# Performance work log

Hardware: AMD Instinct MI355X
Metric: run time of the kernel (lower is better)

Reference implementation:

```python
import jax, jax.numpy as jnp
import numpy as np

B, NQ, NK, D = 8, 2048, 2048, 256


def setup_inputs() -> dict:
    key = jax.random.key(0)
    ks = jax.random.split(key, 4)
    scale = 1.0 / np.sqrt(D)
    return {
        "query": jax.random.normal(ks[0], (B, NQ, D), dtype=jnp.float32),
        "key": jax.random.normal(ks[1], (B, NK, D), dtype=jnp.float32),
        "Wq": jax.random.normal(ks[2], (D, D), dtype=jnp.float32) * scale,
        "bq": jnp.zeros((D,), dtype=jnp.float32),
        "Wk": jax.random.normal(ks[3], (D, D), dtype=jnp.float32) * scale,
        "bk": jnp.zeros((D,), dtype=jnp.float32),
    }


def reference(query, key, Wq, bq, Wk, bk):
    # value = key (pre-projection), as in the torch module
    value = key
    # FFT over the sequence axis (dim=1), keep real part
    q = jnp.real(jnp.fft.fft(query, axis=1)).astype(query.dtype)
    # torch nn.Linear: y = x @ W.T + b
    q = q @ Wq.T + bq                      # [B, NQ, D]
    k = key @ Wk.T + bk                    # [B, NK, D]
    scale = 1.0 / jnp.sqrt(jnp.asarray(q.shape[-1], q.dtype))
    scores = jnp.einsum('bqd,bkd->bqk', q, k) * scale   # [B, NQ, NK]
    probs = jax.nn.softmax(scores, axis=-1)
    out = jnp.einsum('bqk,bkd->bqd', probs, value)       # [B, NQ, D]
    return out
```

## Files before the change

kernel.cpp:

```cpp
#include <hip/hip_runtime.h>

#define B_ 8
#define NQ_ 2048
#define NK_ 2048
#define D_ 256
#define KF_ 1056

typedef __attribute__((ext_vector_type(8))) short bf16x8_t;
typedef __attribute__((ext_vector_type(4))) float f32x4_t;

static __device__ __forceinline__ unsigned short f2bf(float x) {
  unsigned int u = __float_as_uint(x);
  unsigned int r = (u + 0x7FFFu + ((u >> 16) & 1u)) >> 16;
  return (unsigned short)r;
}
static __device__ __forceinline__ float bf2f(unsigned short b) {
  return __uint_as_float(((unsigned int)b) << 16);
}

typedef __attribute__((address_space(1))) unsigned int gas_u32;
typedef __attribute__((address_space(3))) unsigned int las_u32;
static __device__ __forceinline__ void gl16(const void* g, void* l) {
  __builtin_amdgcn_global_load_lds((const gas_u32*)g, (las_u32*)l, 16, 0, 0);
}

__global__ __launch_bounds__(256) void split_kernel(const float* __restrict__ x,
                                                    unsigned short* __restrict__ xh,
                                                    unsigned short* __restrict__ xl,
                                                    int n) {
  const int i = blockIdx.x * 256 + threadIdx.x;
  if (i < n) {
    const float v = x[i];
    const unsigned short hb = f2bf(v);
    xh[i] = hb;
    xl[i] = f2bf(v - bf2f(hb));
  }
}

__global__ __launch_bounds__(256) void cos_split_kernel(unsigned short* __restrict__ Ch,
                                                        unsigned short* __restrict__ Cl) {
  const int idx = blockIdx.x * 256 + threadIdx.x;
  const int i = idx / KF_, n = idx % KF_;
  float c = 0.f;
  if (n <= 1024) {
    const int m = (i * n) & 2047;
    c = cosf((float)m * 0.0030679615757712823f);
  }
  const unsigned short hb = f2bf(c);
  Ch[idx] = hb;
  Cl[idx] = f2bf(c - bf2f(hb));
}

__global__ __launch_bounds__(256) void qtf_split_kernel(const float* __restrict__ q,
                                                        unsigned short* __restrict__ Qtfh,
                                                        unsigned short* __restrict__ Qtfl) {
  __shared__ float lds[32][33];
  const int t  = threadIdx.x;
  const int n0 = blockIdx.x * 32;
  const int d0 = blockIdx.y * 32;
  const int b  = blockIdx.z;
#pragma unroll
  for (int p = 0; p < 4; ++p) {
    const int idx = t + 256 * p;
    const int dd = idx & 31, nn = idx >> 5;
    const int n = n0 + nn;
    float v = 0.f;
    if (n <= 1024) v = q[((size_t)b * NQ_ + n) * D_ + d0 + dd];
    if (n >= 1 && n <= 1023) v += q[((size_t)b * NQ_ + (2048 - n)) * D_ + d0 + dd];
    lds[nn][dd] = v;
  }
  __syncthreads();
#pragma unroll
  for (int p = 0; p < 4; ++p) {
    const int idx = t + 256 * p;
    const int nn = idx & 31, dd = idx >> 5;
    const float v = lds[nn][dd];
    const unsigned short hb = f2bf(v);
    const size_t o = ((size_t)b * D_ + d0 + dd) * KF_ + n0 + nn;
    Qtfh[o] = hb;
    Qtfl[o] = f2bf(v - bf2f(hb));
  }
}

__global__ __launch_bounds__(256) void vt_bf16_kernel(const unsigned short* __restrict__ keyh,
                                                      unsigned short* __restrict__ Vt) {
  __shared__ unsigned short lds[32][40];
  const int t  = threadIdx.x;
  const int j0 = blockIdx.x * 32;
  const int d0 = blockIdx.y * 32;
  const int b  = blockIdx.z;
#pragma unroll
  for (int p = 0; p < 4; ++p) {
    const int idx = t + 256 * p;
    const int dd = idx & 31, jj = idx >> 5;
    lds[jj][dd] = keyh[((size_t)b * NK_ + j0 + jj) * D_ + d0 + dd];
  }
  __syncthreads();
#pragma unroll
  for (int p = 0; p < 4; ++p) {
    const int idx = t + 256 * p;
    const int jj = idx & 31, dd = idx >> 5;
    Vt[((size_t)b * D_ + d0 + dd) * NK_ + j0 + jj] = lds[jj][dd];
  }
}

__global__ __launch_bounds__(256, 2) void dft_mfma(const unsigned short* __restrict__ Ch,
                                                   const unsigned short* __restrict__ Cl,
                                                   const unsigned short* __restrict__ Qtfh,
                                                   const unsigned short* __restrict__ Qtfl,
                                                   float* __restrict__ qr) {
  __shared__ __align__(16) unsigned short Ah[128][40];
  __shared__ __align__(16) unsigned short Al[128][40];
  __shared__ __align__(16) unsigned short Bh[128][40];
  __shared__ __align__(16) unsigned short Bl[128][40];
  const int t = threadIdx.x;
  const int b = blockIdx.z / 3, split = blockIdx.z % 3;
  const int i0 = blockIdx.x * 128, d0 = blockIdx.y * 128;
  const int w = t >> 6, lane = t & 63, quad = lane >> 4, l16 = lane & 15;
  const int wq = w & 1, wj = w >> 1;
  float* qrs = qr + (size_t)split * ((size_t)B_ * 1152 * D_);

  f32x4_t acc[4][4];
#pragma unroll
  for (int a = 0; a < 4; ++a)
#pragma unroll
    for (int c = 0; c < 4; ++c) acc[a][c] = (f32x4_t)0.f;

  const size_t abase = (size_t)i0 * KF_;
  const size_t bbase = ((size_t)b * D_ + d0) * KF_;

  for (int c0 = split * 352; c0 < split * 352 + 352; c0 += 32) {
#pragma unroll
    for (int it = 0; it < 2; ++it) {
      const int unit = t + 256 * it;
      const int row = unit >> 2, u = (unit & 3) * 8;
      const size_t go = (size_t)row * KF_ + c0 + u;
      *(uint4*)&Ah[row][u] = *(const uint4*)&Ch[abase + go];
      *(uint4*)&Al[row][u] = *(const uint4*)&Cl[abase + go];
      *(uint4*)&Bh[row][u] = *(const uint4*)&Qtfh[bbase + go];
      *(uint4*)&Bl[row][u] = *(const uint4*)&Qtfl[bbase + go];
    }
    __syncthreads();
    {
      const int dcol = quad * 8;
      bf16x8_t ah[4], al[4], bh[4], bl[4];
#pragma unroll
      for (int x = 0; x < 4; ++x) {
        ah[x] = *(const bf16x8_t*)&Ah[wq * 64 + x * 16 + l16][dcol];
        al[x] = *(const bf16x8_t*)&Al[wq * 64 + x * 16 + l16][dcol];
        bh[x] = *(const bf16x8_t*)&Bh[wj * 64 + x * 16 + l16][dcol];
        bl[x] = *(const bf16x8_t*)&Bl[wj * 64 + x * 16 + l16][dcol];
      }
#pragma unroll
      for (int at = 0; at < 4; ++at)
#pragma unroll
        for (int jt = 0; jt < 4; ++jt) {
          acc[at][jt] = __builtin_amdgcn_mfma_f32_16x16x32_bf16(ah[at], bh[jt], acc[at][jt], 0, 0, 0);
          acc[at][jt] = __builtin_amdgcn_mfma_f32_16x16x32_bf16(ah[at], bl[jt], acc[at][jt], 0, 0, 0);
          acc[at][jt] = __builtin_amdgcn_mfma_f32_16x16x32_bf16(al[at], bh[jt], acc[at][jt], 0, 0, 0);
        }
    }
    __syncthreads();
  }
#pragma unroll
  for (int at = 0; at < 4; ++at) {
#pragma unroll
    for (int jt = 0; jt < 4; ++jt) {
      const int d = d0 + wj * 64 + jt * 16 + l16;
#pragma unroll
      for (int r = 0; r < 4; ++r) {
        const int i = i0 + wq * 64 + at * 16 + quad * 4 + r;
        qrs[((size_t)b * 1152 + i) * D_ + d] = acc[at][jt][r];
      }
    }
  }
}

__global__ __launch_bounds__(256) void qr_finalize_kernel(const float* __restrict__ qr,
                                                          unsigned short* __restrict__ qrh,
                                                          unsigned short* __restrict__ qrl) {
  const int i = blockIdx.x, b = blockIdx.y, d = threadIdx.x;
  const int src = (i <= 1087) ? i : (2048 - i);
  const size_t S = (size_t)B_ * 1152 * D_;
  const size_t idx = ((size_t)b * 1152 + src) * D_ + d;
  const float v = qr[idx] + qr[idx + S] + qr[idx + 2 * S];
  const unsigned short hb = f2bf(v);
  const size_t o = ((size_t)b * NQ_ + i) * D_ + d;
  qrh[o] = hb;
  qrl[o] = f2bf(v - bf2f(hb));
}

__global__ __launch_bounds__(256, 2) void proj_mfma(const unsigned short* __restrict__ xh,
                                                    const unsigned short* __restrict__ xl,
                                                    const unsigned short* __restrict__ Wh,
                                                    const unsigned short* __restrict__ Wl,
                                                    const float* __restrict__ bias,
                                                    unsigned short* __restrict__ yh,
                                                    unsigned short* __restrict__ yl) {
  __shared__ __align__(16) unsigned short Xh[128][72];
  __shared__ __align__(16) unsigned short Xl[128][72];
  __shared__ __align__(16) unsigned short Bh[128][72];
  __shared__ __align__(16) unsigned short Bl[128][72];
  const int t = threadIdx.x;
  const int m0 = blockIdx.x * 128, o0 = blockIdx.y * 128;
  const int w = t >> 6, lane = t & 63, quad = lane >> 4, l16 = lane & 15;
  const int wq = w & 1, wj = w >> 1;

  f32x4_t acc[4][4];
#pragma unroll
  for (int a = 0; a < 4; ++a)
#pragma unroll
    for (int c = 0; c < 4; ++c) acc[a][c] = (f32x4_t)0.f;

  const size_t xbase = (size_t)m0 * D_;
  const size_t wbase = (size_t)o0 * D_;

  for (int c0 = 0; c0 < D_; c0 += 64) {
#pragma unroll
    for (int it = 0; it < 4; ++it) {
      const int unit = t + 256 * it;
      const int row = unit >> 3, u = (unit & 7) * 8;
      const size_t go = (size_t)row * D_ + c0 + u;
      *(uint4*)&Xh[row][u] = *(const uint4*)&xh[xbase + go];
      *(uint4*)&Xl[row][u] = *(const uint4*)&xl[xbase + go];
      *(uint4*)&Bh[row][u] = *(const uint4*)&Wh[wbase + go];
      *(uint4*)&Bl[row][u] = *(const uint4*)&Wl[wbase + go];
    }
    __syncthreads();
#pragma unroll
    for (int ks = 0; ks < 2; ++ks) {
      const int dcol = ks * 32 + quad * 8;
      bf16x8_t ah[4], al[4], bh[4], bl[4];
#pragma unroll
      for (int x = 0; x < 4; ++x) {
        ah[x] = *(const bf16x8_t*)&Xh[wq * 64 + x * 16 + l16][dcol];
        al[x] = *(const bf16x8_t*)&Xl[wq * 64 + x * 16 + l16][dcol];
        bh[x] = *(const bf16x8_t*)&Bh[wj * 64 + x * 16 + l16][dcol];
        bl[x] = *(const bf16x8_t*)&Bl[wj * 64 + x * 16 + l16][dcol];
      }
#pragma unroll
      for (int at = 0; at < 4; ++at)
#pragma unroll
        for (int jt = 0; jt < 4; ++jt) {
          acc[at][jt] = __builtin_amdgcn_mfma_f32_16x16x32_bf16(ah[at], bh[jt], acc[at][jt], 0, 0, 0);
          acc[at][jt] = __builtin_amdgcn_mfma_f32_16x16x32_bf16(ah[at], bl[jt], acc[at][jt], 0, 0, 0);
          acc[at][jt] = __builtin_amdgcn_mfma_f32_16x16x32_bf16(al[at], bh[jt], acc[at][jt], 0, 0, 0);
        }
    }
    __syncthreads();
  }
#pragma unroll
  for (int at = 0; at < 4; ++at) {
#pragma unroll
    for (int jt = 0; jt < 4; ++jt) {
      const int o = o0 + wj * 64 + jt * 16 + l16;
      const float bv = bias[o];
#pragma unroll
      for (int r = 0; r < 4; ++r) {
        const int m = m0 + wq * 64 + at * 16 + quad * 4 + r;
        const float v = acc[at][jt][r] + bv;
        const unsigned short hb = f2bf(v);
        yh[(size_t)m * D_ + o] = hb;
        yl[(size_t)m * D_ + o] = f2bf(v - bf2f(hb));
      }
    }
  }
}

__global__ __launch_bounds__(512, 4) void scores_p(const unsigned short* __restrict__ qh,
                                                   const unsigned short* __restrict__ ql,
                                                   const unsigned short* __restrict__ kh,
                                                   const unsigned short* __restrict__ kl,
                                                   unsigned short* __restrict__ Pb,
                                                   float2* __restrict__ stat) {
  __shared__ __align__(16) unsigned short Qh[128][64];
  __shared__ __align__(16) unsigned short Ql[128][64];
  __shared__ __align__(16) unsigned short Kh[128][64];
  __shared__ __align__(16) unsigned short Kl[128][64];
  __shared__ float mred[2][128];
  __shared__ float lred[2][128];
  const int t = threadIdx.x;
  const int b = blockIdx.z;
  const int i0 = blockIdx.x * 128, j0 = blockIdx.y * 128;
  const int jb = blockIdx.y;
  const int w = t >> 6, lane = t & 63, quad = lane >> 4, l16 = lane & 15;
  const int wq = w & 3, wj = w >> 2;
  const int sr0 = t >> 3, ssl = t & 7;

  f32x4_t acc[2][4];
#pragma unroll
  for (int x = 0; x < 2; ++x)
#pragma unroll
    for (int y = 0; y < 4; ++y) acc[x][y] = (f32x4_t)0.f;

  const size_t qbase = ((size_t)b * NQ_ + i0) * D_;
  const size_t kbase = ((size_t)b * NK_ + j0) * D_;

  auto STAGE = [&](int c0) {
#pragma unroll
    for (int half = 0; half < 2; ++half) {
      const int row = half * 64 + sr0;
      const int sg = (ssl ^ (row & 7)) * 8;
      const size_t ro = (size_t)row * D_ + c0 + sg;
      gl16(qh + qbase + ro, &Qh[half * 64 + w * 8][0]);
      gl16(ql + qbase + ro, &Ql[half * 64 + w * 8][0]);
      gl16(kh + kbase + ro, &Kh[half * 64 + w * 8][0]);
      gl16(kl + kbase + ro, &Kl[half * 64 + w * 8][0]);
    }
  };

  STAGE(0);

#pragma unroll
  for (int s = 0; s < 4; ++s) {
    asm volatile("s_waitcnt vmcnt(0)" ::: "memory");
    __builtin_amdgcn_s_barrier();
    asm volatile("" ::: "memory");

#pragma unroll
    for (int ks = 0; ks < 2; ++ks) {
      bf16x8_t ah[2], al[2], bh[4], bl[4];
#pragma unroll
      for (int x = 0; x < 2; ++x) {
        const int ar = wq * 32 + x * 16 + l16;
        const int asl = ((ks * 4 + quad) ^ (ar & 7)) * 8;
        ah[x] = *(const bf16x8_t*)&Qh[ar][asl];
        al[x] = *(const bf16x8_t*)&Ql[ar][asl];
      }
#pragma unroll
      for (int y = 0; y < 4; ++y) {
        const int br = wj * 64 + y * 16 + l16;
        const int bsl = ((ks * 4 + quad) ^ (br & 7)) * 8;
        bh[y] = *(const bf16x8_t*)&Kh[br][bsl];
        bl[y] = *(const bf16x8_t*)&Kl[br][bsl];
      }
#pragma unroll
      for (int x = 0; x < 2; ++x)
#pragma unroll
        for (int y = 0; y < 4; ++y) {
          acc[x][y] = __builtin_amdgcn_mfma_f32_16x16x32_bf16(ah[x], bh[y], acc[x][y], 0, 0, 0);
          acc[x][y] = __builtin_amdgcn_mfma_f32_16x16x32_bf16(ah[x], bl[y], acc[x][y], 0, 0, 0);
          acc[x][y] = __builtin_amdgcn_mfma_f32_16x16x32_bf16(al[x], bh[y], acc[x][y], 0, 0, 0);
        }
    }

    asm volatile("" ::: "memory");
    __builtin_amdgcn_s_barrier();
    asm volatile("" ::: "memory");
    if (s < 3) STAGE((s + 1) * 64);
  }

  const float scale = 0.0625f;
  float mt[2][4];
#pragma unroll
  for (int x = 0; x < 2; ++x)
#pragma unroll
    for (int r = 0; r < 4; ++r) mt[x][r] = -3e38f;
#pragma unroll
  for (int x = 0; x < 2; ++x)
#pragma unroll
    for (int y = 0; y < 4; ++y)
#pragma unroll
      for (int r = 0; r < 4; ++r) {
        acc[x][y][r] *= scale;
        mt[x][r] = fmaxf(mt[x][r], acc[x][y][r]);
      }
#pragma unroll
  for (int off = 1; off < 16; off <<= 1)
#pragma unroll
    for (int x = 0; x < 2; ++x)
#pragma unroll
      for (int r = 0; r < 4; ++r) mt[x][r] = fmaxf(mt[x][r], __shfl_xor(mt[x][r], off));
  if (l16 == 0) {
#pragma unroll
    for (int x = 0; x < 2; ++x)
#pragma unroll
      for (int r = 0; r < 4; ++r)
        mred[wj][wq * 32 + x * 16 + quad * 4 + r] = mt[x][r];
  }
  __syncthreads();
  float nrow[2][4], mu[2][4], lt[2][4];
#pragma unroll
  for (int x = 0; x < 2; ++x)
#pragma unroll
    for (int r = 0; r < 4; ++r) {
      const int rr = wq * 32 + x * 16 + quad * 4 + r;
      const float m = fmaxf(mred[0][rr], mred[1][rr]);
      const float n = ceilf(m * 1.44269504f);
      nrow[x][r] = n;
      mu[x][r] = n * 0.69314718056f;
      lt[x][r] = 0.f;
    }
  const size_t pbase = ((size_t)(b * 16 + jb)) * NQ_ * 128;
#pragma unroll
  for (int x = 0; x < 2; ++x)
#pragma unroll
    for (int y = 0; y < 4; ++y) {
      const int jloc = wj * 64 + y * 16 + l16;
#pragma unroll
      for (int r = 0; r < 4; ++r) {
        const int i = i0 + wq * 32 + x * 16 + quad * 4 + r;
        float p = __expf(acc[x][y][r] - mu[x][r]);
        p = fmaxf(p, 8.673617e-19f);
        lt[x][r] += p;
        Pb[pbase + (size_t)i * 128 + jloc] = f2bf(p);
      }
    }
#pragma unroll
  for (int off = 1; off < 16; off <<= 1)
#pragma unroll
    for (int x = 0; x < 2; ++x)
#pragma unroll
      for (int r = 0; r < 4; ++r) lt[x][r] += __shfl_xor(lt[x][r], off);
  if (l16 == 0) {
#pragma unroll
    for (int x = 0; x < 2; ++x)
#pragma unroll
      for (int r = 0; r < 4; ++r)
        lred[wj][wq * 32 + x * 16 + quad * 4 + r] = lt[x][r];
  }
  __syncthreads();
  if (wj == 0 && l16 == 0) {
#pragma unroll
    for (int x = 0; x < 2; ++x)
#pragma unroll
      for (int r = 0; r < 4; ++r) {
        const int rr = wq * 32 + x * 16 + quad * 4 + r;
        stat[(size_t)jb * (B_ * NQ_) + (size_t)b * NQ_ + i0 + rr] =
            make_float2(nrow[x][r], lred[0][rr] + lred[1][rr]);
      }
  }
}

__global__ __launch_bounds__(256) void rowfin_kernel(const float2* __restrict__ stat,
                                                     float2* __restrict__ srow) {
  const int i = blockIdx.x * 256 + threadIdx.x;
  float2 st[16];
  float m = -3e38f;
#pragma unroll
  for (int jb = 0; jb < 16; ++jb) {
    st[jb] = stat[(size_t)jb * (B_ * NQ_) + i];
    m = fmaxf(m, st[jb].x);
  }
  float l = 0.f;
#pragma unroll
  for (int jb = 0; jb < 16; ++jb) l += st[jb].y * exp2f(st[jb].x - m);
  srow[i] = make_float2(m, 1.0f / l);
}

__global__ __launch_bounds__(512, 1) void pv_p(const unsigned short* __restrict__ Pb,
                                               const float2* __restrict__ stat,
                                               const float2* __restrict__ srow,
                                               const unsigned short* __restrict__ Vt,
                                               float* __restrict__ out) {
  __shared__ __align__(16) unsigned short Ps[3][64][64];
  __shared__ __align__(16) unsigned short Vs[3][256][64];
  const int t = threadIdx.x;
  const int lb = (blockIdx.x & 7) * 32 + (blockIdx.x >> 3);
  const int mb = lb * 64;
  const int b  = lb >> 5;
  const int i0 = mb & (NQ_ - 1);
  const int w = t >> 6, lane = t & 63, quad = lane >> 4, l16 = lane & 15;
  const int wm = w & 1, wd = w >> 1;
  const int prow = t >> 3, pslot = t & 7;

  unsigned int es2[16][2];
  {
    float nmax[2];
#pragma unroll
    for (int x = 0; x < 2; ++x)
      nmax[x] = srow[mb + wm * 32 + x * 16 + l16].x;
#pragma unroll
    for (int jb = 0; jb < 16; ++jb)
#pragma unroll
      for (int x = 0; x < 2; ++x) {
        const int arow = mb + wm * 32 + x * 16 + l16;
        int e = (int)(nmax[x] - stat[(size_t)jb * (B_ * NQ_) + arow].x);
        e = e < 0 ? 0 : (e > 60 ? 60 : e);
        es2[jb][x] = (unsigned int)(e << 7) * 0x00010001u;
      }
  }

  f32x4_t acc[2][4];
#pragma unroll
  for (int x = 0; x < 2; ++x)
#pragma unroll
    for (int y = 0; y < 4; ++y) acc[x][y] = (f32x4_t)0.f;

  const size_t vbase = (size_t)b * D_ * (size_t)NK_;

  auto STAGE = [&](int nb, int s) {
    const int jj = s * 64;
    const int jb = jj >> 7, off = jj & 127;
    {
      const int sg = pslot ^ (prow & 7);
      gl16(Pb + ((size_t)(b * 16 + jb)) * NQ_ * 128 +
               (size_t)(i0 + prow) * 128 + off + sg * 8,
           &Ps[nb][w * 8][0]);
    }
#pragma unroll
    for (int k = 0; k < 4; ++k) {
      const int vrow = k * 64 + prow;
      const int sg = pslot ^ (vrow & 7);
      gl16(Vt + vbase + (size_t)vrow * NK_ + jj + sg * 8,
           &Vs[nb][k * 64 + w * 8][0]);
    }
  };

  asm volatile("s_waitcnt vmcnt(0)" ::: "memory");
  STAGE(0, 0);
  STAGE(1, 1);

#pragma unroll
  for (int s = 0; s < 32; ++s) {
    const int cb = s % 3;
    if (s < 30) {
      STAGE((s + 2) % 3, s + 2);
      asm volatile("s_waitcnt vmcnt(10)" ::: "memory");
    } else if (s == 30) {
      asm volatile("s_waitcnt vmcnt(5)" ::: "memory");
    } else {
      asm volatile("s_waitcnt vmcnt(0)" ::: "memory");
    }
    __builtin_amdgcn_s_barrier();
    asm volatile("" ::: "memory");

    const unsigned int e0 = es2[s >> 1][0], e1 = es2[s >> 1][1];
#pragma unroll
    for (int ks = 0; ks < 2; ++ks) {
      bf16x8_t a[2], bv[4];
#pragma unroll
      for (int x = 0; x < 2; ++x) {
        const int row = wm * 32 + x * 16 + l16;
        const int sk = (ks * 4 + quad) ^ (row & 7);
        uint4 u = *(const uint4*)&Ps[cb][row][sk * 8];
        const unsigned int e = (x == 0) ? e0 : e1;
        u.x -= e; u.y -= e; u.z -= e; u.w -= e;
        a[x] = *(const bf16x8_t*)&u;
      }
#pragma unroll
      for (int y = 0; y < 4; ++y) {
        const int row = wd * 64 + y * 16 + l16;
        const int sk = (ks * 4 + quad) ^ (row & 7);
        bv[y] = *(const bf16x8_t*)&Vs[cb][row][sk * 8];
      }
#pragma unroll
      for (int x = 0; x < 2; ++x)
#pragma unroll
        for (int y = 0; y < 4; ++y)
          acc[x][y] = __builtin_amdgcn_mfma_f32_16x16x32_bf16(a[x], bv[y], acc[x][y], 0, 0, 0);
    }

    asm volatile("" ::: "memory");
    __builtin_amdgcn_s_barrier();
    asm volatile("" ::: "memory");
  }

#pragma unroll
  for (int x = 0; x < 2; ++x) {
    float sy[4];
#pragma unroll
    for (int r = 0; r < 4; ++r)
      sy[r] = srow[mb + wm * 32 + x * 16 + quad * 4 + r].y;
#pragma unroll
    for (int y = 0; y < 4; ++y) {
      const int d = wd * 64 + y * 16 + l16;
#pragma unroll
      for (int r = 0; r < 4; ++r) {
        const int m = mb + wm * 32 + x * 16 + quad * 4 + r;
        out[(size_t)m * D_ + d] = acc[x][y][r] * sy[r];
      }
    }
  }
}

extern "C" void kernel_launch(void* const* d_in, const int* in_sizes, int n_in,
                              void* d_out, int out_size, void* d_ws, size_t ws_size,
                              hipStream_t stream) {
  const float* query = (const float*)d_in[0];
  const float* key   = (const float*)d_in[1];
  const float* Wq    = (const float*)d_in[2];
  const float* bq    = (const float*)d_in[3];
  const float* Wk    = (const float*)d_in[4];
  const float* bk    = (const float*)d_in[5];
  float* out = (float*)d_out;

  char* ws = (char*)d_ws;
  const size_t MB = (size_t)1 << 20;
  unsigned short* qh = (unsigned short*)(ws);
  unsigned short* ql = (unsigned short*)(ws + 8 * MB);
  unsigned short* kh = (unsigned short*)(ws + 16 * MB);
  unsigned short* kl = (unsigned short*)(ws + 24 * MB);
  unsigned short* Vt = (unsigned short*)(ws + 32 * MB);
  unsigned short* Pb = (unsigned short*)(ws + 40 * MB);
  float2* stat = (float2*)(ws + 108 * MB);
  float2* srow = (float2*)(ws + 110 * MB);
  unsigned short* Ch   = (unsigned short*)(ws + 40 * MB);
  unsigned short* Cl   = (unsigned short*)(ws + 43 * MB);
  unsigned short* Qtfh = (unsigned short*)(ws + 46 * MB);
  unsigned short* Qtfl = (unsigned short*)(ws + 51 * MB);
  float*          qr   = (float*)(ws + 56 * MB);
  unsigned short* qrh  = (unsigned short*)(ws + 40 * MB);
  unsigned short* qrl  = (unsigned short*)(ws + 48 * MB);
  unsigned short* keyh = (unsigned short*)(ws + 92 * MB);
  unsigned short* keyl = (unsigned short*)(ws + 100 * MB);
  unsigned short* Wqh  = (unsigned short*)(ws + 111 * MB);
  unsigned short* Wql  = (unsigned short*)(ws + 111 * MB + 256 * 1024);
  unsigned short* Wkh  = (unsigned short*)(ws + 111 * MB + 512 * 1024);
  unsigned short* Wkl  = (unsigned short*)(ws + 111 * MB + 768 * 1024);

  dim3 blk(256);

  split_kernel<<<B_ * NK_ * D_ / 256, blk, 0, stream>>>(key, keyh, keyl, B_ * NK_ * D_);
  split_kernel<<<D_ * D_ / 256, blk, 0, stream>>>(Wq, Wqh, Wql, D_ * D_);
  split_kernel<<<D_ * D_ / 256, blk, 0, stream>>>(Wk, Wkh, Wkl, D_ * D_);
  cos_split_kernel<<<1152 * KF_ / 256, blk, 0, stream>>>(Ch, Cl);
  qtf_split_kernel<<<dim3(KF_ / 32, D_ / 32, B_), blk, 0, stream>>>(query, Qtfh, Qtfl);
  dft_mfma<<<dim3(9, 2, B_ * 3), blk, 0, stream>>>(Ch, Cl, Qtfh, Qtfl, qr);
  qr_finalize_kernel<<<dim3(2048, B_), blk, 0, stream>>>(qr, qrh, qrl);
  proj_mfma<<<dim3(B_ * NQ_ / 128, 2), blk, 0, stream>>>(qrh, qrl, Wqh, Wql, bq, qh, ql);
  proj_mfma<<<dim3(B_ * NK_ / 128, 2), blk, 0, stream>>>(keyh, keyl, Wkh, Wkl, bk, kh, kl);
  vt_bf16_kernel<<<dim3(NK_ / 32, D_ / 32, B_), blk, 0, stream>>>(keyh, Vt);
  scores_p<<<dim3(NQ_ / 128, NK_ / 128, B_), dim3(512), 0, stream>>>(qh, ql, kh, kl, Pb, stat);
  rowfin_kernel<<<B_ * NQ_ / 256, blk, 0, stream>>>(stat, srow);
  pv_p<<<dim3(256), dim3(512), 0, stream>>>(Pb, stat, srow, Vt, out);
}
```

Baseline: 206.7 us.

## Widen scores tile to 128x256 with interleaved hi/lo LDS staging

The scores kernel now computes a 128x256 tile per block instead of 128x128, halving the grid along the key axis. Each wave owns a 64x64 sub-tile with 16 accumulators, which raises MFMA work per LDS fragment load. The hi and lo bf16 halves are packed into one swizzled LDS row, and the K dimension is staged in 32-wide chunks over 8 steps. Statistics are still written per 128-column block so downstream kernels are unchanged. The larger tile increases register pressure under launch_bounds(512,4), which may spill or lower occupancy, and the grid shrinks to 1024 blocks.

```diff
diff --git a/kernel.cpp b/kernel.cpp
--- a/kernel.cpp
+++ b/kernel.cpp
@@ -273,161 +273,157 @@
                                                    const unsigned short* __restrict__ kl,
                                                    unsigned short* __restrict__ Pb,
                                                    float2* __restrict__ stat) {
-  __shared__ __align__(16) unsigned short Qh[128][64];
-  __shared__ __align__(16) unsigned short Ql[128][64];
-  __shared__ __align__(16) unsigned short Kh[128][64];
-  __shared__ __align__(16) unsigned short Kl[128][64];
-  __shared__ float mred[2][128];
-  __shared__ float lred[2][128];
+  __shared__ __align__(16) unsigned short Qhl[128][64];
+  __shared__ __align__(16) unsigned short Khl[256][64];
+  __shared__ float mred[4][128];
+  __shared__ float lred[4][128];
   const int t = threadIdx.x;
   const int b = blockIdx.z;
-  const int i0 = blockIdx.x * 128, j0 = blockIdx.y * 128;
-  const int jb = blockIdx.y;
+  const int i0 = blockIdx.x * 128, j0 = blockIdx.y * 256;
+  const int jb0 = blockIdx.y * 2;
   const int w = t >> 6, lane = t & 63, quad = lane >> 4, l16 = lane & 15;
-  const int wq = w & 3, wj = w >> 2;
-  const int sr0 = t >> 3, ssl = t & 7;
-
-  f32x4_t acc[2][4];
-#pragma unroll
-  for (int x = 0; x < 2; ++x)
-#pragma unroll
-    for (int y = 0; y < 4; ++y) acc[x][y] = (f32x4_t)0.f;
+  const int wq = w & 1, wj = w >> 1;
+  const int jbl = wj >> 1;
+
+  f32x4_t acc[4][4];
+#pragma unroll
+  for (int a = 0; a < 4; ++a)
+#pragma unroll
+    for (int c = 0; c < 4; ++c) acc[a][c] = (f32x4_t)0.f;
 
   const size_t qbase = ((size_t)b * NQ_ + i0) * D_;
   const size_t kbase = ((size_t)b * NK_ + j0) * D_;
 
   auto STAGE = [&](int c0) {
 #pragma unroll
-    for (int half = 0; half < 2; ++half) {
-      const int row = half * 64 + sr0;
-      const int sg = (ssl ^ (row & 7)) * 8;
-      const size_t ro = (size_t)row * D_ + c0 + sg;
-      gl16(qh + qbase + ro, &Qh[half * 64 + w * 8][0]);
-      gl16(ql + qbase + ro, &Ql[half * 64 + w * 8][0]);
-      gl16(kh + kbase + ro, &Kh[half * 64 + w * 8][0]);
-      gl16(kl + kbase + ro, &Kl[half * 64 + w * 8][0]);
+    for (int cp = 0; cp < 2; ++cp) {
+      const int r = w * 16 + cp * 8 + (lane >> 3);
+      const int lg = (lane & 7) ^ (r & 7);
+      const unsigned short* src = (lg < 4) ? qh : ql;
+      gl16(src + qbase + (size_t)r * D_ + c0 + (lg & 3) * 8,
+           &Qhl[w * 16 + cp * 8][0]);
+    }
+#pragma unroll
+    for (int cp = 0; cp < 4; ++cp) {
+      const int r = w * 32 + cp * 8 + (lane >> 3);
+      const int lg = (lane & 7) ^ (r & 7);
+      const unsigned short* src = (lg < 4) ? kh : kl;
+      gl16(src + kbase + (size_t)r * D_ + c0 + (lg & 3) * 8,
+           &Khl[w * 32 + cp * 8][0]);
     }
   };
 
   STAGE(0);
 
 #pragma unroll
-  for (int s = 0; s < 4; ++s) {
+  for (int s = 0; s < 8; ++s) {
     asm volatile("s_waitcnt vmcnt(0)" ::: "memory");
     __builtin_amdgcn_s_barrier();
     asm volatile("" ::: "memory");
 
-#pragma unroll
-    for (int ks = 0; ks < 2; ++ks) {
-      bf16x8_t ah[2], al[2], bh[4], bl[4];
-#pragma unroll
-      for (int x = 0; x < 2; ++x) {
-        const int ar = wq * 32 + x * 16 + l16;
-        const int asl = ((ks * 4 + quad) ^ (ar & 7)) * 8;
-        ah[x] = *(const bf16x8_t*)&Qh[ar][asl];
-        al[x] = *(const bf16x8_t*)&Ql[ar][asl];
-      }
-#pragma unroll
-      for (int y = 0; y < 4; ++y) {
-        const int br = wj * 64 + y * 16 + l16;
-        const int bsl = ((ks * 4 + quad) ^ (br & 7)) * 8;
-        bh[y] = *(const bf16x8_t*)&Kh[br][bsl];
-        bl[y] = *(const bf16x8_t*)&Kl[br][bsl];
-      }
-#pragma unroll
-      for (int x = 0; x < 2; ++x)
-#pragma unroll
-        for (int y = 0; y < 4; ++y) {
-          acc[x][y] = __builtin_amdgcn_mfma_f32_16x16x32_bf16(ah[x], bh[y], acc[x][y], 0, 0, 0);
-          acc[x][y] = __builtin_amdgcn_mfma_f32_16x16x32_bf16(ah[x], bl[y], acc[x][y], 0, 0, 0);
-          acc[x][y] = __builtin_amdgcn_mfma_f32_16x16x32_bf16(al[x], bh[y], acc[x][y], 0, 0, 0);
-        }
-    }
+    bf16x8_t ah[4], al[4], bh[4], bl[4];
+#pragma unroll
+    for (int x = 0; x < 4; ++x) {
+      const int ar = wq * 64 + x * 16 + l16;
+      ah[x] = *(const bf16x8_t*)&Qhl[ar][(quad ^ (ar & 7)) * 8];
+      al[x] = *(const bf16x8_t*)&Qhl[ar][((4 + quad) ^ (ar & 7)) * 8];
+      const int br = wj * 64 + x * 16 + l16;
+      bh[x] = *(const bf16x8_t*)&Khl[br][(quad ^ (br & 7)) * 8];
+      bl[x] = *(const bf16x8_t*)&Khl[br][((4 + quad) ^ (br & 7)) * 8];
+    }
+#pragma unroll
+    for (int at = 0; at < 4; ++at)
+#pragma unroll
+      for (int jt = 0; jt < 4; ++jt) {
+        acc[at][jt] = __builtin_amdgcn_mfma_f32_16x16x32_bf16(ah[at], bh[jt], acc[at][jt], 0, 0, 0);
+        acc[at][jt] = __builtin_amdgcn_mfma_f32_16x16x32_bf16(ah[at], bl[jt], acc[at][jt], 0, 0, 0);
+        acc[at][jt] = __builtin_amdgcn_mfma_f32_16x16x32_bf16(al[at], bh[jt], acc[at][jt], 0, 0, 0);
+      }
 
     asm volatile("" ::: "memory");
     __builtin_amdgcn_s_barrier();
     asm volatile("" ::: "memory");
-    if (s < 3) STAGE((s + 1) * 64);
+    if (s < 7) STAGE((s + 1) * 32);
   }
 
   const float scale = 0.0625f;
-  float mt[2][4];
-#pragma unroll
-  for (int x = 0; x < 2; ++x)
-#pragma unroll
-    for (int r = 0; r < 4; ++r) mt[x][r] = -3e38f;
-#pragma unroll
-  for (int x = 0; x < 2; ++x)
-#pragma unroll
-    for (int y = 0; y < 4; ++y)
+  float mt[4][4];
+#pragma unroll
+  for (int at = 0; at < 4; ++at)
+#pragma unroll
+    for (int r = 0; r < 4; ++r) mt[at][r] = -3e38f;
+#pragma unroll
+  for (int at = 0; at < 4; ++at)
+#pragma unroll
+    for (int jt = 0; jt < 4; ++jt)
 #pragma unroll
       for (int r = 0; r < 4; ++r) {
-        acc[x][y][r] *= scale;
-        mt[x][r] = fmaxf(mt[x][r], acc[x][y][r]);
+        acc[at][jt][r] *= scale;
+        mt[at][r] = fmaxf(mt[at][r], acc[at][jt][r]);
       }
 #pragma unroll
   for (int off = 1; off < 16; off <<= 1)
 #pragma unroll
-    for (int x = 0; x < 2; ++x)
-#pragma unroll
-      for (int r = 0; r < 4; ++r) mt[x][r] = fmaxf(mt[x][r], __shfl_xor(mt[x][r], off));
+    for (int at = 0; at < 4; ++at)
+#pragma unroll
+      for (int r = 0; r < 4; ++r) mt[at][r] = fmaxf(mt[at][r], __shfl_xor(mt[at][r], off));
   if (l16 == 0) {
 #pragma unroll
-    for (int x = 0; x < 2; ++x)
+    for (int at = 0; at < 4; ++at)
 #pragma unroll
       for (int r = 0; r < 4; ++r)
-        mred[wj][wq * 32 + x * 16 + quad * 4 + r] = mt[x][r];
+        mred[wj][wq * 64 + at * 16 + quad * 4 + r] = mt[at][r];
   }
   __syncthreads();
-  float nrow[2][4], mu[2][4], lt[2][4];
-#pragma unroll
-  for (int x = 0; x < 2; ++x)
+  float nrow[4][4], mu[4][4], lt[4][4];
+#pragma unroll
+  for (int at = 0; at < 4; ++at)
 #pragma unroll
     for (int r = 0; r < 4; ++r) {
-      const int rr = wq * 32 + x * 16 + quad * 4 + r;
-      const float m = fmaxf(mred[0][rr], mred[1][rr]);
+      const int rr = wq * 64 + at * 16 + quad * 4 + r;
+      const float m = fmaxf(mred[jbl * 2][rr], mred[jbl * 2 + 1][rr]);
       const float n = ceilf(m * 1.44269504f);
-      nrow[x][r] = n;
-      mu[x][r] = n * 0.69314718056f;
-      lt[x][r] = 0.f;
-    }
-  const size_t pbase = ((size_t)(b * 16 + jb)) * NQ_ * 128;
-#pragma unroll
-  for (int x = 0; x < 2; ++x)
-#pragma unroll
-    for (int y = 0; y < 4; ++y) {
-      const int jloc = wj * 64 + y * 16 + l16;
+      nrow[at][r] = n;
+      mu[at][r] = n * 0.69314718056f;
+      lt[at][r] = 0.f;
+    }
+  const size_t pbase = ((size_t)(b * 16 + jb0 + jbl)) * NQ_ * 128;
+#pragma unroll
+  for (int at = 0; at < 4; ++at)
+#pragma unroll
+    for (int jt = 0; jt < 4; ++jt) {
+      const int jloc = (wj & 1) * 64 + jt * 16 + l16;
 #pragma unroll
       for (int r = 0; r < 4; ++r) {
-        const int i = i0 + wq * 32 + x * 16 + quad * 4 + r;
-        float p = __expf(acc[x][y][r] - mu[x][r]);
+        const int i = i0 + wq * 64 + at * 16 + quad * 4 + r;
+        float p = __expf(acc[at][jt][r] - mu[at][r]);
         p = fmaxf(p, 8.673617e-19f);
-        lt[x][r] += p;
+        lt[at][r] += p;
         Pb[pbase + (size_t)i * 128 + jloc] = f2bf(p);
       }
     }
 #pragma unroll
   for (int off = 1; off < 16; off <<= 1)
 #pragma unroll
-    for (int x = 0; x < 2; ++x)
-#pragma unroll
-      for (int r = 0; r < 4; ++r) lt[x][r] += __shfl_xor(lt[x][r], off);
+    for (int at = 0; at < 4; ++at)
+#pragma unroll
+      for (int r = 0; r < 4; ++r) lt[at][r] += __shfl_xor(lt[at][r], off);
   if (l16 == 0) {
 #pragma unroll
-    for (int x = 0; x < 2; ++x)
+    for (int at = 0; at < 4; ++at)
 #pragma unroll
       for (int r = 0; r < 4; ++r)
-        lred[wj][wq * 32 + x * 16 + quad * 4 + r] = lt[x][r];
+        lred[wj][wq * 64 + at * 16 + quad * 4 + r] = lt[at][r];
   }
   __syncthreads();
-  if (wj == 0 && l16 == 0) {
-#pragma unroll
-    for (int x = 0; x < 2; ++x)
+  if ((wj & 1) == 0 && l16 == 0) {
+#pragma unroll
+    for (int at = 0; at < 4; ++at)
 #pragma unroll
       for (int r = 0; r < 4; ++r) {
-        const int rr = wq * 32 + x * 16 + quad * 4 + r;
-        stat[(size_t)jb * (B_ * NQ_) + (size_t)b * NQ_ + i0 + rr] =
-            make_float2(nrow[x][r], lred[0][rr] + lred[1][rr]);
+        const int rr = wq * 64 + at * 16 + quad * 4 + r;
+        stat[(size_t)(jb0 + jbl) * (B_ * NQ_) + (size_t)b * NQ_ + i0 + rr] =
+            make_float2(nrow[at][r], lred[jbl * 2][rr] + lred[jbl * 2 + 1][rr]);
       }
   }
 }
@@ -621,7 +617,7 @@
   proj_mfma<<<dim3(B_ * NQ_ / 128, 2), blk, 0, stream>>>(qrh, qrl, Wqh, Wql, bq, qh, ql);
   proj_mfma<<<dim3(B_ * NK_ / 128, 2), blk, 0, stream>>>(keyh, keyl, Wkh, Wkl, bk, kh, kl);
   vt_bf16_kernel<<<dim3(NK_ / 32, D_ / 32, B_), blk, 0, stream>>>(keyh, Vt);
-  scores_p<<<dim3(NQ_ / 128, NK_ / 128, B_), dim3(512), 0, stream>>>(qh, ql, kh, kl, Pb, stat);
+  scores_p<<<dim3(NQ_ / 128, NK_ / 256, B_), dim3(512), 0, stream>>>(qh, ql, kh, kl, Pb, stat);
   rowfin_kernel<<<B_ * NQ_ / 256, blk, 0, stream>>>(stat, srow);
   pv_p<<<dim3(256), dim3(512), 0, stream>>>(Pb, stat, srow, Vt, out);
 }
```

Result: no change. 207.0 us (+0.1%).
